# Kernel tuning notes

Hardware: AMD Instinct MI355X
Metric: run time of the kernel (lower is better)

Reference implementation:

```python
import jax, jax.numpy as jnp
import numpy as np

DIM = 256
NUM_HEADS = 8
HEAD_DIM = DIM // NUM_HEADS
NUM_MAIN = 2
NUM_MOD = 4
SEQ_MAIN = 1536
SEQ_AUX = 768
BS = 2


def setup_inputs() -> dict:
    key = jax.random.key(0)
    ks = jax.random.split(key, 6)
    x0 = jax.random.normal(ks[0], (BS, SEQ_MAIN, DIM), jnp.float32)
    x1 = jax.random.normal(ks[1], (BS, SEQ_MAIN, DIM), jnp.float32)
    x2 = jax.random.normal(ks[2], (BS, SEQ_AUX, DIM), jnp.float32)
    x3 = jax.random.normal(ks[3], (BS, SEQ_AUX, DIM), jnp.float32)
    Wqkv = jax.random.normal(ks[4], (NUM_MOD, DIM, 3 * DIM), jnp.float32) * 0.02
    bqkv = jnp.zeros((NUM_MOD, 3 * DIM), jnp.float32)
    Wproj = jax.random.normal(ks[5], (NUM_MOD, DIM, DIM), jnp.float32) * 0.02
    bproj = jnp.zeros((NUM_MOD, DIM), jnp.float32)
    return {"x0": x0, "x1": x1, "x2": x2, "x3": x3,
            "Wqkv": Wqkv, "bqkv": bqkv, "Wproj": Wproj, "bproj": bproj}


def _split_qkv(qkv):
    bs, s, _ = qkv.shape
    qkv = qkv.reshape(bs, s, 3, NUM_HEADS, HEAD_DIM).transpose(2, 0, 3, 1, 4)
    return qkv[0], qkv[1], qkv[2]


def _sdpa(q, k, v):
    scale = 1.0 / jnp.sqrt(jnp.asarray(HEAD_DIM, q.dtype))
    scores = jnp.einsum('bhqd,bhkd->bhqk', q, k) * scale
    probs = jax.nn.softmax(scores, axis=-1)
    return jnp.einsum('bhqk,bhkd->bhqd', probs, v)


def _merge_heads(t):
    # [bs, heads, s, head_dim] -> [bs, s, dim]
    bs, h, s, d = t.shape
    return t.transpose(0, 2, 1, 3).reshape(bs, s, h * d)


def reference(x0, x1, x2, x3, Wqkv, bqkv, Wproj, bproj):
    xs = [x0, x1, x2, x3]
    seqlens = [x.shape[1] for x in xs]
    qs, ks, vs = [], [], []
    for i in range(NUM_MOD):
        q, k, v = _split_qkv(xs[i] @ Wqkv[i] + bqkv[i])
        qs.append(q); ks.append(k); vs.append(v)

    main_q = jnp.concatenate(qs[:NUM_MAIN], axis=2)
    main_k = jnp.concatenate(ks[:NUM_MAIN], axis=2)
    main_v = jnp.concatenate(vs[:NUM_MAIN], axis=2)
    main_x = _merge_heads(_sdpa(main_q, main_k, main_v))  # [bs, sum(main seqlens), dim]
    splits = np.cumsum(seqlens[:NUM_MAIN])[:-1]
    outs = list(jnp.split(main_x, splits, axis=1))

    # aux modalities attend over detached main KV + own KV
    mk = jax.lax.stop_gradient(main_k)
    mv = jax.lax.stop_gradient(main_v)
    for i in range(NUM_MAIN, NUM_MOD):
        k = jnp.concatenate([mk, ks[i]], axis=2)
        v = jnp.concatenate([mv, vs[i]], axis=2)
        outs.append(_merge_heads(_sdpa(qs[i], k, v)))

    outs = [outs[i] @ Wproj[i] + bproj[i] for i in range(NUM_MOD)]
    # concatenate per-modality outputs along the sequence dim for a single output
    return jnp.concatenate(outs, axis=1)
```

## Files before the change

### kernel.cpp

```cpp
#include <hip/hip_runtime.h>
#include <hip/hip_bf16.h>
#include <math.h>

#define BS 2
#define NHEADS 8
#define HD 32
#define DIM 256
#define W3 768
#define S_MAIN 1536
#define S_AUX 768
#define SM_TOT 3072
#define S_TOT 4608

typedef _Float16 f16x8 __attribute__((ext_vector_type(8)));
typedef _Float16 f16x4 __attribute__((ext_vector_type(4)));
typedef float    f32x4 __attribute__((ext_vector_type(4)));

#define QK_SCALE 0.25503491f

#define QM_H  0
#define KM_H  1572864
#define VMT_H 3145728
#define QA_H  4718592
#define KA_H  5505024
#define VAT_H 6291456
#define AO0_F 3538944
#define AO1_F 5898240
#define L0_F  8257536
#define L1_F  8266752

#define GLOAD_LDS(SRC, DST)                                                    \
    __builtin_amdgcn_global_load_lds(                                          \
        (const __attribute__((address_space(1))) void*)(SRC),                  \
        (__attribute__((address_space(3))) void*)(DST), 16, 0, 0)

__global__ __launch_bounds__(256) void qkv_mfma_kernel(
    const float* __restrict__ x0, const float* __restrict__ x1,
    const float* __restrict__ x2, const float* __restrict__ x3,
    const float* __restrict__ Wqkv, const float* __restrict__ bqkv,
    _Float16* __restrict__ wsh)
{
    const int m  = blockIdx.z;
    const int rt = blockIdx.y;
    const int ct = blockIdx.x;
    const int s_m   = (m < 2) ? S_MAIN : S_AUX;
    const int nrows = BS * s_m;
    const int r0 = rt * 128;
    if (r0 >= nrows) return;

    const float* x    = (m == 0) ? x0 : (m == 1) ? x1 : (m == 2) ? x2 : x3;
    const float* W    = Wqkv + m * (DIM * W3);
    const float* bias = bqkv + m * W3;

    __shared__ _Float16 As[128][40];
    __shared__ _Float16 Bs[64][40];

    const int t    = threadIdx.x;
    const int wid  = t >> 6;
    const int lane = t & 63;
    const int g    = lane >> 4;
    const int c    = lane & 15;
    const int c0   = ct * 64;

    const int arow = t >> 1;
    const int ak   = (t & 1) << 4;
    const int bcol = t & 63;
    const int bkg  = t >> 6;
    const int bsg  = bkg ^ ((bcol >> 3) & 3);

    f32x4 acc[2][4];
    #pragma unroll
    for (int i = 0; i < 2; ++i)
        #pragma unroll
        for (int j = 0; j < 4; ++j)
            acc[i][j] = (f32x4){0.f, 0.f, 0.f, 0.f};

    const float* xp = x + (r0 + arow) * DIM + ak;
    const float* wp = W + (bkg * 8) * W3 + c0 + bcol;

    for (int kk = 0; kk < DIM; kk += 32) {
        {
            const float4 u0 = *(const float4*)(xp + kk + 0);
            const float4 u1 = *(const float4*)(xp + kk + 4);
            const float4 u2 = *(const float4*)(xp + kk + 8);
            const float4 u3 = *(const float4*)(xp + kk + 12);
            f16x8 h0, h1;
            h0[0] = (_Float16)u0.x; h0[1] = (_Float16)u0.y;
            h0[2] = (_Float16)u0.z; h0[3] = (_Float16)u0.w;
            h0[4] = (_Float16)u1.x; h0[5] = (_Float16)u1.y;
            h0[6] = (_Float16)u1.z; h0[7] = (_Float16)u1.w;
            h1[0] = (_Float16)u2.x; h1[1] = (_Float16)u2.y;
            h1[2] = (_Float16)u2.z; h1[3] = (_Float16)u2.w;
            h1[4] = (_Float16)u3.x; h1[5] = (_Float16)u3.y;
            h1[6] = (_Float16)u3.z; h1[7] = (_Float16)u3.w;
            *(f16x8*)&As[arow][ak]     = h0;
            *(f16x8*)&As[arow][ak + 8] = h1;
        }
        {
            const float* wq = wp + kk * W3;
            f16x8 hb;
            hb[0] = (_Float16)wq[0 * W3]; hb[1] = (_Float16)wq[1 * W3];
            hb[2] = (_Float16)wq[2 * W3]; hb[3] = (_Float16)wq[3 * W3];
            hb[4] = (_Float16)wq[4 * W3]; hb[5] = (_Float16)wq[5 * W3];
            hb[6] = (_Float16)wq[6 * W3]; hb[7] = (_Float16)wq[7 * W3];
            *(f16x8*)&Bs[bcol][bsg << 3] = hb;
        }
        __syncthreads();
        const f16x8 af0 = *(const f16x8*)&As[wid * 32 + c][g * 8];
        const f16x8 af1 = *(const f16x8*)&As[wid * 32 + 16 + c][g * 8];
        #pragma unroll
        for (int j = 0; j < 4; ++j) {
            const int bc = j * 16 + c;
            const int gg = g ^ ((bc >> 3) & 3);
            const f16x8 bf = *(const f16x8*)&Bs[bc][gg * 8];
            acc[0][j] = __builtin_amdgcn_mfma_f32_16x16x32_f16(af0, bf, acc[0][j], 0, 0, 0);
            acc[1][j] = __builtin_amdgcn_mfma_f32_16x16x32_f16(af1, bf, acc[1][j], 0, 0, 0);
        }
        __syncthreads();
    }

    #pragma unroll
    for (int i = 0; i < 2; ++i) {
        const int gr = r0 + wid * 32 + i * 16 + 4 * g;
        const int b  = (gr >= s_m) ? 1 : 0;
        const int s  = gr - (b ? s_m : 0);
        #pragma unroll
        for (int j = 0; j < 4; ++j) {
            const int col   = c0 + j * 16 + c;
            const int which = col >> 8;
            const int head  = (col >> 5) & 7;
            const int dd    = col & 31;
            const float bv  = bias[col];
            const f32x4 a   = acc[i][j];
            if (which < 2) {
                const float qs = (which == 0) ? QK_SCALE : 1.0f;
                _Float16* dst;
                int base;
                if (m < 2) {
                    dst  = wsh + (which == 0 ? QM_H : KM_H);
                    base = ((b * NHEADS + head) * SM_TOT + (s + m * S_MAIN)) * HD + dd;
                } else {
                    dst  = wsh + (which == 0 ? QA_H : KA_H);
                    base = ((((m - 2) * BS + b) * NHEADS + head) * S_AUX + s) * HD + dd;
                }
                dst[base + 0 * HD] = (_Float16)((a[0] + bv) * qs);
                dst[base + 1 * HD] = (_Float16)((a[1] + bv) * qs);
                dst[base + 2 * HD] = (_Float16)((a[2] + bv) * qs);
                dst[base + 3 * HD] = (_Float16)((a[3] + bv) * qs);
            } else {
                _Float16* dst;
                int base;
                if (m < 2) {
                    dst  = wsh + VMT_H;
                    base = ((b * NHEADS + head) * HD + dd) * SM_TOT + (s + m * S_MAIN);
                } else {
                    dst  = wsh + VAT_H;
                    base = ((((m - 2) * BS + b) * NHEADS + head) * HD + dd) * S_AUX + s;
                }
                f16x4 hv;
                hv[0] = (_Float16)(a[0] + bv);
                hv[1] = (_Float16)(a[1] + bv);
                hv[2] = (_Float16)(a[2] + bv);
                hv[3] = (_Float16)(a[3] + bv);
                *(f16x4*)(dst + base) = hv;
            }
        }
    }
}

__global__ __launch_bounds__(256) void attn_mfma_kernel(
    const _Float16* __restrict__ wsh, float* __restrict__ wsf)
{
    __shared__ _Float16 kbuf[2][64 * 32];
    __shared__ _Float16 vbuf[2][32 * 64];

    const int wid  = threadIdx.x >> 6;
    const int lane = threadIdx.x & 63;
    const int g    = lane >> 4;
    const int c    = lane & 15;

    const int bid = blockIdx.x;

    const _Float16 *qp, *kp0, *vt0, *kp1, *vt1;
    int n0, n1, vs1, orow0, ocol, half;

    if (bid < 384) {
        const int mbhg = bid / 12;
        const int mod  = mbhg >> 4;
        const int b    = (mbhg >> 3) & 1;
        const int h    = mbhg & 7;
        const int t    = bid % 12;
        const int qt   = t >> 1;
        half = t & 1;
        const int q0   = qt * 128 + wid * 32;
        const int mbh  = (mod * BS + b) * NHEADS + h;
        const int bh   = b * NHEADS + h;
        qp = wsh + QA_H + (mbh * S_AUX + q0) * HD;
        if (half == 0) {
            kp0 = wsh + KM_H  + bh * SM_TOT * HD;
            vt0 = wsh + VMT_H + bh * HD * SM_TOT;
            n0  = 1920;
            kp1 = nullptr; vt1 = nullptr; n1 = 0; vs1 = 0;
        } else {
            kp0 = wsh + KM_H  + (bh * SM_TOT + 1920) * HD;
            vt0 = wsh + VMT_H + bh * HD * SM_TOT + 1920;
            n0  = 1152;
            kp1 = wsh + KA_H  + mbh * S_AUX * HD;
            vt1 = wsh + VAT_H + mbh * HD * S_AUX;
            n1  = S_AUX; vs1 = S_AUX;
        }
        orow0 = b * S_TOT + SM_TOT + mod * S_AUX + q0;
        ocol  = h * HD;
    } else {
        const int idx = bid - 384;
        const int bh  = idx / 48;
        const int t   = idx % 48;
        const int qt  = t >> 1;
        half = t & 1;
        const int q0  = qt * 128 + wid * 32;
        const int b = bh >> 3, h = bh & 7;
        const int ks = half * 1536;
        qp  = wsh + QM_H  + (bh * SM_TOT + q0) * HD;
        kp0 = wsh + KM_H  + (bh * SM_TOT + ks) * HD;
        vt0 = wsh + VMT_H + bh * HD * SM_TOT + ks;
        n0  = 1536;
        kp1 = nullptr; vt1 = nullptr; n1 = 0; vs1 = 0;
        orow0 = b * S_TOT + q0;
        ocol  = h * HD;
    }

    const f16x8 qfA = *(const f16x8*)(qp + c * HD + g * 8);
    const f16x8 qfB = *(const f16x8*)(qp + (16 + c) * HD + g * 8);

    const int pc    = ((c >> 2) << 3) + (c & 3);
    const int koff0 = pc * HD + g * 8;
    const int koff1 = (pc + 4) * HD + g * 8;

    const int srow = wid * 8 + (lane >> 3);
    const int jl   = lane & 7;
    const int vswz = (jl ^ (srow & 7)) << 3;
    const int vr0 = ((g     ^ (c & 7)) << 3);
    const int vr1 = (((g+4) ^ (c & 7)) << 3);

    f16x8 ones;
    #pragma unroll
    for (int i = 0; i < 8; ++i) ones[i] = (_Float16)1.0f;

    f32x4 otA0 = {0.f, 0.f, 0.f, 0.f}, otA1 = {0.f, 0.f, 0.f, 0.f};
    f32x4 otB0 = {0.f, 0.f, 0.f, 0.f}, otB1 = {0.f, 0.f, 0.f, 0.f};
    f32x4 ltA  = {0.f, 0.f, 0.f, 0.f}, ltB  = {0.f, 0.f, 0.f, 0.f};

    int cur = 0;

    #pragma unroll 1
    for (int seg = 0; seg < 2; ++seg) {
        const _Float16* kp_ = seg ? kp1 : kp0;
        const _Float16* vt_ = seg ? vt1 : vt0;
        const int n  = seg ? n1  : n0;
        const int vs = seg ? vs1 : SM_TOT;
        if (n == 0) break;

        #define STAGE(BI, K0)                                                  \
            {                                                                  \
                const _Float16* ks_ = kp_ + (K0) * HD + wid * 512 + lane * 8;  \
                GLOAD_LDS(ks_, &kbuf[BI][wid * 512]);                          \
                const _Float16* vs_ = vt_ + (K0) + srow * vs + vswz;           \
                GLOAD_LDS(vs_, &vbuf[BI][wid * 512]);                          \
            }

        #define COMPUTE_TILE(BI)                                               \
            {                                                                  \
                const _Float16* kb_ = &kbuf[BI][0];                            \
                const _Float16* vb_ = &vbuf[BI][0];                            \
                const f16x8 kf0 = *(const f16x8*)(kb_ + koff0);                \
                const f16x8 kf1 = *(const f16x8*)(kb_ + koff1);                \
                const f16x8 kf2 = *(const f16x8*)(kb_ + 32 * HD + koff0);      \
                const f16x8 kf3 = *(const f16x8*)(kb_ + 32 * HD + koff1);      \
                const f16x8 va0 = *(const f16x8*)(vb_ + c * 64 + vr0);         \
                const f16x8 va1 = *(const f16x8*)(vb_ + (16 + c) * 64 + vr0);  \
                const f16x8 vb0 = *(const f16x8*)(vb_ + c * 64 + vr1);         \
                const f16x8 vb1 = *(const f16x8*)(vb_ + (16 + c) * 64 + vr1);  \
                f32x4 sA0 = __builtin_amdgcn_mfma_f32_16x16x32_f16(            \
                    kf0, qfA, (f32x4){0.f, 0.f, 0.f, 0.f}, 0, 0, 0);           \
                f32x4 sA1 = __builtin_amdgcn_mfma_f32_16x16x32_f16(            \
                    kf1, qfA, (f32x4){0.f, 0.f, 0.f, 0.f}, 0, 0, 0);           \
                f32x4 sA2 = __builtin_amdgcn_mfma_f32_16x16x32_f16(            \
                    kf2, qfA, (f32x4){0.f, 0.f, 0.f, 0.f}, 0, 0, 0);           \
                f32x4 sA3 = __builtin_amdgcn_mfma_f32_16x16x32_f16(            \
                    kf3, qfA, (f32x4){0.f, 0.f, 0.f, 0.f}, 0, 0, 0);           \
                f32x4 sB0 = __builtin_amdgcn_mfma_f32_16x16x32_f16(            \
                    kf0, qfB, (f32x4){0.f, 0.f, 0.f, 0.f}, 0, 0, 0);           \
                f32x4 sB1 = __builtin_amdgcn_mfma_f32_16x16x32_f16(            \
                    kf1, qfB, (f32x4){0.f, 0.f, 0.f, 0.f}, 0, 0, 0);           \
                f32x4 sB2 = __builtin_amdgcn_mfma_f32_16x16x32_f16(            \
                    kf2, qfB, (f32x4){0.f, 0.f, 0.f, 0.f}, 0, 0, 0);           \
                f32x4 sB3 = __builtin_amdgcn_mfma_f32_16x16x32_f16(            \
                    kf3, qfB, (f32x4){0.f, 0.f, 0.f, 0.f}, 0, 0, 0);           \
                float pA0[4], pA1[4], pA2[4], pA3[4];                          \
                float pB0[4], pB1[4], pB2[4], pB3[4];                          \
                _Pragma("unroll")                                              \
                for (int r = 0; r < 4; ++r) {                                  \
                    pA0[r] = __builtin_amdgcn_exp2f(sA0[r]);                   \
                    pA1[r] = __builtin_amdgcn_exp2f(sA1[r]);                   \
                    pA2[r] = __builtin_amdgcn_exp2f(sA2[r]);                   \
                    pA3[r] = __builtin_amdgcn_exp2f(sA3[r]);                   \
                    pB0[r] = __builtin_amdgcn_exp2f(sB0[r]);                   \
                    pB1[r] = __builtin_amdgcn_exp2f(sB1[r]);                   \
                    pB2[r] = __builtin_amdgcn_exp2f(sB2[r]);                   \
                    pB3[r] = __builtin_amdgcn_exp2f(sB3[r]);                   \
                }                                                              \
                f16x8 pbA0, pbA1, pbB0, pbB1;                                  \
                _Pragma("unroll")                                              \
                for (int r = 0; r < 4; ++r) {                                  \
                    pbA0[r]     = (_Float16)pA0[r];                            \
                    pbA0[r + 4] = (_Float16)pA1[r];                            \
                    pbA1[r]     = (_Float16)pA2[r];                            \
                    pbA1[r + 4] = (_Float16)pA3[r];                            \
                    pbB0[r]     = (_Float16)pB0[r];                            \
                    pbB0[r + 4] = (_Float16)pB1[r];                            \
                    pbB1[r]     = (_Float16)pB2[r];                            \
                    pbB1[r + 4] = (_Float16)pB3[r];                            \
                }                                                              \
                ltA = __builtin_amdgcn_mfma_f32_16x16x32_f16(ones, pbA0, ltA, 0, 0, 0); \
                ltA = __builtin_amdgcn_mfma_f32_16x16x32_f16(ones, pbA1, ltA, 0, 0, 0); \
                ltB = __builtin_amdgcn_mfma_f32_16x16x32_f16(ones, pbB0, ltB, 0, 0, 0); \
                ltB = __builtin_amdgcn_mfma_f32_16x16x32_f16(ones, pbB1, ltB, 0, 0, 0); \
                otA0 = __builtin_amdgcn_mfma_f32_16x16x32_f16(va0, pbA0, otA0, 0, 0, 0); \
                otA1 = __builtin_amdgcn_mfma_f32_16x16x32_f16(va1, pbA0, otA1, 0, 0, 0); \
                otB0 = __builtin_amdgcn_mfma_f32_16x16x32_f16(va0, pbB0, otB0, 0, 0, 0); \
                otB1 = __builtin_amdgcn_mfma_f32_16x16x32_f16(va1, pbB0, otB1, 0, 0, 0); \
                otA0 = __builtin_amdgcn_mfma_f32_16x16x32_f16(vb0, pbA1, otA0, 0, 0, 0); \
                otA1 = __builtin_amdgcn_mfma_f32_16x16x32_f16(vb1, pbA1, otA1, 0, 0, 0); \
                otB0 = __builtin_amdgcn_mfma_f32_16x16x32_f16(vb0, pbB1, otB0, 0, 0, 0); \
                otB1 = __builtin_amdgcn_mfma_f32_16x16x32_f16(vb1, pbB1, otB1, 0, 0, 0); \
            }

        STAGE(cur, 0);
        __syncthreads();

        #pragma unroll 1
        for (int k0 = 0; k0 < n; k0 += 64) {
            if (k0 + 64 < n)
                STAGE(cur ^ 1, k0 + 64);
            COMPUTE_TILE(cur);
            __syncthreads();
            cur ^= 1;
        }

        #undef STAGE
        #undef COMPUTE_TILE
    }

    float* aoBase = wsf + (half ? AO1_F : AO0_F);
    float* lBase  = wsf + (half ? L1_F  : L0_F);

    float* aoA = aoBase + (orow0 + c) * DIM + ocol;
    float* aoB = aoBase + (orow0 + 16 + c) * DIM + ocol;
    float4 w0, w1, w2, w3;
    w0.x = otA0[0]; w0.y = otA0[1]; w0.z = otA0[2]; w0.w = otA0[3];
    w1.x = otA1[0]; w1.y = otA1[1]; w1.z = otA1[2]; w1.w = otA1[3];
    w2.x = otB0[0]; w2.y = otB0[1]; w2.z = otB0[2]; w2.w = otB0[3];
    w3.x = otB1[0]; w3.y = otB1[1]; w3.z = otB1[2]; w3.w = otB1[3];
    *(float4*)(aoA + 4 * g)      = w0;
    *(float4*)(aoA + 16 + 4 * g) = w1;
    *(float4*)(aoB + 4 * g)      = w2;
    *(float4*)(aoB + 16 + 4 * g) = w3;

    if (g == 0) {
        lBase[orow0 + c]      = ltA[0];
        lBase[orow0 + 16 + c] = ltB[0];
    }
}

__global__ __launch_bounds__(256) void proj_mfma_kernel(
    const float* __restrict__ wsf, const float* __restrict__ Wproj,
    const float* __restrict__ bproj, float* __restrict__ out)
{
    const int ct = blockIdx.x;
    const int rt = blockIdx.y;
    const int r0 = rt * 128, c0 = ct * 64;
    const int seq = r0 % S_TOT;
    const int mod = (seq < S_MAIN) ? 0 : (seq < SM_TOT) ? 1
                  : (seq < SM_TOT + S_AUX) ? 2 : 3;
    const float* W    = Wproj + mod * DIM * DIM;
    const float* bias = bproj + mod * DIM;
    const float* A0   = wsf + AO0_F;
    const float* A1   = wsf + AO1_F;
    const float* L0p  = wsf + L0_F;
    const float* L1p  = wsf + L1_F;

    __shared__ _Float16 As[128][40];
    __shared__ _Float16 Bs[64][40];
    __shared__ float Linv[128];

    const int t    = threadIdx.x;
    const int wid  = t >> 6;
    const int lane = t & 63;
    const int g    = lane >> 4;
    const int c    = lane & 15;

    if (t < 128) Linv[t] = 1.0f / (L0p[r0 + t] + L1p[r0 + t]);
    __syncthreads();

    const int arow = t >> 1;
    const int ak   = (t & 1) << 4;
    const int bcol = t & 63;
    const int bkg  = t >> 6;
    const int bsg  = bkg ^ ((bcol >> 3) & 3);
    const float linv_r = Linv[arow];

    f32x4 acc[2][4];
    #pragma unroll
    for (int i = 0; i < 2; ++i)
        #pragma unroll
        for (int j = 0; j < 4; ++j)
            acc[i][j] = (f32x4){0.f, 0.f, 0.f, 0.f};

    const float* pa0 = A0 + (r0 + arow) * DIM + ak;
    const float* pa1 = A1 + (r0 + arow) * DIM + ak;
    const float* wp  = W + (bkg * 8) * DIM + c0 + bcol;

    for (int kk = 0; kk < DIM; kk += 32) {
        {
            const float4 u0 = *(const float4*)(pa0 + kk + 0);
            const float4 u1 = *(const float4*)(pa0 + kk + 4);
            const float4 u2 = *(const float4*)(pa0 + kk + 8);
            const float4 u3 = *(const float4*)(pa0 + kk + 12);
            const float4 v0 = *(const float4*)(pa1 + kk + 0);
            const float4 v1 = *(const float4*)(pa1 + kk + 4);
            const float4 v2 = *(const float4*)(pa1 + kk + 8);
            const float4 v3 = *(const float4*)(pa1 + kk + 12);
            f16x8 h0, h1;
            h0[0] = (_Float16)((u0.x + v0.x) * linv_r);
            h0[1] = (_Float16)((u0.y + v0.y) * linv_r);
            h0[2] = (_Float16)((u0.z + v0.z) * linv_r);
            h0[3] = (_Float16)((u0.w + v0.w) * linv_r);
            h0[4] = (_Float16)((u1.x + v1.x) * linv_r);
            h0[5] = (_Float16)((u1.y + v1.y) * linv_r);
            h0[6] = (_Float16)((u1.z + v1.z) * linv_r);
            h0[7] = (_Float16)((u1.w + v1.w) * linv_r);
            h1[0] = (_Float16)((u2.x + v2.x) * linv_r);
            h1[1] = (_Float16)((u2.y + v2.y) * linv_r);
            h1[2] = (_Float16)((u2.z + v2.z) * linv_r);
            h1[3] = (_Float16)((u2.w + v2.w) * linv_r);
            h1[4] = (_Float16)((u3.x + v3.x) * linv_r);
            h1[5] = (_Float16)((u3.y + v3.y) * linv_r);
            h1[6] = (_Float16)((u3.z + v3.z) * linv_r);
            h1[7] = (_Float16)((u3.w + v3.w) * linv_r);
            *(f16x8*)&As[arow][ak]     = h0;
            *(f16x8*)&As[arow][ak + 8] = h1;
        }
        {
            const float* wq = wp + kk * DIM;
            f16x8 hb;
            hb[0] = (_Float16)wq[0 * DIM]; hb[1] = (_Float16)wq[1 * DIM];
            hb[2] = (_Float16)wq[2 * DIM]; hb[3] = (_Float16)wq[3 * DIM];
            hb[4] = (_Float16)wq[4 * DIM]; hb[5] = (_Float16)wq[5 * DIM];
            hb[6] = (_Float16)wq[6 * DIM]; hb[7] = (_Float16)wq[7 * DIM];
            *(f16x8*)&Bs[bcol][bsg << 3] = hb;
        }
        __syncthreads();
        const f16x8 af0 = *(const f16x8*)&As[wid * 32 + c][g * 8];
        const f16x8 af1 = *(const f16x8*)&As[wid * 32 + 16 + c][g * 8];
        #pragma unroll
        for (int j = 0; j < 4; ++j) {
            const int bc = j * 16 + c;
            const int gg = g ^ ((bc >> 3) & 3);
            const f16x8 bf = *(const f16x8*)&Bs[bc][gg * 8];
            acc[0][j] = __builtin_amdgcn_mfma_f32_16x16x32_f16(af0, bf, acc[0][j], 0, 0, 0);
            acc[1][j] = __builtin_amdgcn_mfma_f32_16x16x32_f16(af1, bf, acc[1][j], 0, 0, 0);
        }
        __syncthreads();
    }

    #pragma unroll
    for (int i = 0; i < 2; ++i) {
        const int gr = r0 + wid * 32 + i * 16 + 4 * g;
        #pragma unroll
        for (int j = 0; j < 4; ++j) {
            const int col  = c0 + j * 16 + c;
            const float bv = bias[col];
            const f32x4 a  = acc[i][j];
            out[(gr + 0) * DIM + col] = a[0] + bv;
            out[(gr + 1) * DIM + col] = a[1] + bv;
            out[(gr + 2) * DIM + col] = a[2] + bv;
            out[(gr + 3) * DIM + col] = a[3] + bv;
        }
    }
}

extern "C" void kernel_launch(void* const* d_in, const int* in_sizes, int n_in,
                              void* d_out, int out_size, void* d_ws, size_t ws_size,
                              hipStream_t stream)
{
    const float* x0    = (const float*)d_in[0];
    const float* x1    = (const float*)d_in[1];
    const float* x2    = (const float*)d_in[2];
    const float* x3    = (const float*)d_in[3];
    const float* Wqkv  = (const float*)d_in[4];
    const float* bqkv  = (const float*)d_in[5];
    const float* Wproj = (const float*)d_in[6];
    const float* bproj = (const float*)d_in[7];
    _Float16* wsh = (_Float16*)d_ws;
    float*    wsf = (float*)d_ws;
    float*    out = (float*)d_out;

    qkv_mfma_kernel<<<dim3(12, 24, 4), 256, 0, stream>>>(
        x0, x1, x2, x3, Wqkv, bqkv, wsh);

    attn_mfma_kernel<<<dim3(1152), 256, 0, stream>>>(wsh, wsf);

    proj_mfma_kernel<<<dim3(4, 72), 256, 0, stream>>>(wsf, Wproj, bproj, out);
}
```

Before: 95.72 us.

## Pre-convert inputs and transpose weights to fp16, swizzle K tile loads in attention

Adds a conversion kernel that casts the activations to fp16 and writes transposed fp16 copies of the QKV and projection weights into workspace. The QKV and projection GEMMs then issue contiguous 16-byte fp16 loads in place of strided scalar fp32 weight reads and in-loop conversions. The attention kernel also applies an XOR swizzle to K tile staging to reduce LDS bank conflicts. In exchange it costs an extra kernel launch and an extra pass over x and the weights through global memory, and the weight transpose loop writes scalar fp16 values with a strided pattern.

```diff
diff --git a/kernel.cpp b/kernel.cpp
--- a/kernel.cpp
+++ b/kernel.cpp
@@ -24,20 +24,77 @@
 #define QA_H  4718592
 #define KA_H  5505024
 #define VAT_H 6291456
+#define XH_H  7077888
 #define AO0_F 3538944
 #define AO1_F 5898240
 #define L0_F  8257536
 #define L1_F  8266752
+#define WT1_H 16551936
+#define WT2_H 17338368
 
 #define GLOAD_LDS(SRC, DST)                                                    \
     __builtin_amdgcn_global_load_lds(                                          \
         (const __attribute__((address_space(1))) void*)(SRC),                  \
         (__attribute__((address_space(3))) void*)(DST), 16, 0, 0)
 
-__global__ __launch_bounds__(256) void qkv_mfma_kernel(
+__global__ __launch_bounds__(256) void convert_kernel(
     const float* __restrict__ x0, const float* __restrict__ x1,
     const float* __restrict__ x2, const float* __restrict__ x3,
-    const float* __restrict__ Wqkv, const float* __restrict__ bqkv,
+    const float* __restrict__ Wqkv, const float* __restrict__ Wproj,
+    _Float16* __restrict__ wsh)
+{
+    const int bid = blockIdx.x;
+    const int t   = threadIdx.x;
+
+    if (bid < 1152) {
+        const float* src;
+        int off;
+        if (bid < 384)      { src = x0; off = (bid      ) * 2048; }
+        else if (bid < 768) { src = x1 - 786432 + 0;  off = bid * 2048; }
+        else if (bid < 960) { src = x2; off = 1572864 + (bid - 768) * 2048; }
+        else                { src = x3; off = 1966080 + (bid - 960) * 2048; }
+        const int base = (bid < 384) ? bid * 2048
+                       : (bid < 768) ? (bid - 384) * 2048
+                       : (bid < 960) ? (bid - 768) * 2048
+                       : (bid - 960) * 2048;
+        const float* p = ((bid < 384) ? x0 : (bid < 768) ? x1
+                         : (bid < 960) ? x2 : x3) + base + t * 8;
+        _Float16* dst = wsh + XH_H + off + t * 8;
+        const float4 u0 = *(const float4*)(p + 0);
+        const float4 u1 = *(const float4*)(p + 4);
+        f16x8 h;
+        h[0] = (_Float16)u0.x; h[1] = (_Float16)u0.y;
+        h[2] = (_Float16)u0.z; h[3] = (_Float16)u0.w;
+        h[4] = (_Float16)u1.x; h[5] = (_Float16)u1.y;
+        h[6] = (_Float16)u1.z; h[7] = (_Float16)u1.w;
+        *(f16x8*)dst = h;
+    } else if (bid < 1200) {
+        const int i  = bid - 1152;
+        const int m  = i / 12;
+        const int cc = i % 12;
+        const int col = cc * 64 + (t & 63);
+        const int kq  = t >> 6;
+        const float* Wm = Wqkv + m * (DIM * W3);
+        _Float16*   Wt  = wsh + WT1_H + m * (W3 * DIM) + col * DIM;
+        #pragma unroll 4
+        for (int k = kq * 64; k < kq * 64 + 64; ++k)
+            Wt[k] = (_Float16)Wm[k * W3 + col];
+    } else {
+        const int i  = bid - 1200;
+        const int m  = i / 4;
+        const int cc = i % 4;
+        const int col = cc * 64 + (t & 63);
+        const int kq  = t >> 6;
+        const float* Wm = Wproj + m * (DIM * DIM);
+        _Float16*   Wt  = wsh + WT2_H + m * (DIM * DIM) + col * DIM;
+        #pragma unroll 4
+        for (int k = kq * 64; k < kq * 64 + 64; ++k)
+            Wt[k] = (_Float16)Wm[k * DIM + col];
+    }
+}
+
+__global__ __launch_bounds__(256) void qkv_mfma_kernel(
+    const _Float16* __restrict__ wsh_ro, const float* __restrict__ bqkv,
     _Float16* __restrict__ wsh)
 {
     const int m  = blockIdx.z;
@@ -48,9 +105,11 @@
     const int r0 = rt * 128;
     if (r0 >= nrows) return;
 
-    const float* x    = (m == 0) ? x0 : (m == 1) ? x1 : (m == 2) ? x2 : x3;
-    const float* W    = Wqkv + m * (DIM * W3);
-    const float* bias = bqkv + m * W3;
+    const int xoff = (m == 0) ? 0 : (m == 1) ? 786432
+                   : (m == 2) ? 1572864 : 1966080;
+    const _Float16* xh = wsh_ro + XH_H + xoff;
+    const _Float16* Wt = wsh_ro + WT1_H + m * (W3 * DIM);
+    const float* bias  = bqkv + m * W3;
 
     __shared__ _Float16 As[128][40];
     __shared__ _Float16 Bs[64][40];
@@ -75,34 +134,18 @@
         for (int j = 0; j < 4; ++j)
             acc[i][j] = (f32x4){0.f, 0.f, 0.f, 0.f};
 
-    const float* xp = x + (r0 + arow) * DIM + ak;
-    const float* wp = W + (bkg * 8) * W3 + c0 + bcol;
+    const _Float16* xp = xh + (r0 + arow) * DIM + ak;
+    const _Float16* wp = Wt + (c0 + bcol) * DIM;
 
     for (int kk = 0; kk < DIM; kk += 32) {
         {
-            const float4 u0 = *(const float4*)(xp + kk + 0);
-            const float4 u1 = *(const float4*)(xp + kk + 4);
-            const float4 u2 = *(const float4*)(xp + kk + 8);
-            const float4 u3 = *(const float4*)(xp + kk + 12);
-            f16x8 h0, h1;
-            h0[0] = (_Float16)u0.x; h0[1] = (_Float16)u0.y;
-            h0[2] = (_Float16)u0.z; h0[3] = (_Float16)u0.w;
-            h0[4] = (_Float16)u1.x; h0[5] = (_Float16)u1.y;
-            h0[6] = (_Float16)u1.z; h0[7] = (_Float16)u1.w;
-            h1[0] = (_Float16)u2.x; h1[1] = (_Float16)u2.y;
-            h1[2] = (_Float16)u2.z; h1[3] = (_Float16)u2.w;
-            h1[4] = (_Float16)u3.x; h1[5] = (_Float16)u3.y;
-            h1[6] = (_Float16)u3.z; h1[7] = (_Float16)u3.w;
+            const f16x8 h0 = *(const f16x8*)(xp + kk);
+            const f16x8 h1 = *(const f16x8*)(xp + kk + 8);
             *(f16x8*)&As[arow][ak]     = h0;
             *(f16x8*)&As[arow][ak + 8] = h1;
         }
         {
-            const float* wq = wp + kk * W3;
-            f16x8 hb;
-            hb[0] = (_Float16)wq[0 * W3]; hb[1] = (_Float16)wq[1 * W3];
-            hb[2] = (_Float16)wq[2 * W3]; hb[3] = (_Float16)wq[3 * W3];
-            hb[4] = (_Float16)wq[4 * W3]; hb[5] = (_Float16)wq[5 * W3];
-            hb[6] = (_Float16)wq[6 * W3]; hb[7] = (_Float16)wq[7 * W3];
+            const f16x8 hb = *(const f16x8*)(wp + kk + bkg * 8);
             *(f16x8*)&Bs[bcol][bsg << 3] = hb;
         }
         __syncthreads();
@@ -233,8 +276,12 @@
     const f16x8 qfB = *(const f16x8*)(qp + (16 + c) * HD + g * 8);
 
     const int pc    = ((c >> 2) << 3) + (c & 3);
-    const int koff0 = pc * HD + g * 8;
-    const int koff1 = (pc + 4) * HD + g * 8;
+    const int kchr  = (g ^ (c >> 2)) << 3;
+    const int koff0 = pc * HD + kchr;
+    const int koff1 = (pc + 4) * HD + kchr;
+
+    const int krow  = wid * 16 + (lane >> 2);
+    const int kchg  = ((lane & 3) ^ ((krow >> 3) & 3)) << 3;
 
     const int srow = wid * 8 + (lane >> 3);
     const int jl   = lane & 7;
@@ -262,7 +309,7 @@
 
         #define STAGE(BI, K0)                                                  \
             {                                                                  \
-                const _Float16* ks_ = kp_ + (K0) * HD + wid * 512 + lane * 8;  \
+                const _Float16* ks_ = kp_ + (K0 + krow) * HD + kchg;           \
                 GLOAD_LDS(ks_, &kbuf[BI][wid * 512]);                          \
                 const _Float16* vs_ = vt_ + (K0) + srow * vs + vswz;           \
                 GLOAD_LDS(vs_, &vbuf[BI][wid * 512]);                          \
@@ -373,7 +420,7 @@
 }
 
 __global__ __launch_bounds__(256) void proj_mfma_kernel(
-    const float* __restrict__ wsf, const float* __restrict__ Wproj,
+    const float* __restrict__ wsf, const _Float16* __restrict__ wsh_ro,
     const float* __restrict__ bproj, float* __restrict__ out)
 {
     const int ct = blockIdx.x;
@@ -382,12 +429,12 @@
     const int seq = r0 % S_TOT;
     const int mod = (seq < S_MAIN) ? 0 : (seq < SM_TOT) ? 1
                   : (seq < SM_TOT + S_AUX) ? 2 : 3;
-    const float* W    = Wproj + mod * DIM * DIM;
-    const float* bias = bproj + mod * DIM;
-    const float* A0   = wsf + AO0_F;
-    const float* A1   = wsf + AO1_F;
-    const float* L0p  = wsf + L0_F;
-    const float* L1p  = wsf + L1_F;
+    const _Float16* Wt = wsh_ro + WT2_H + mod * (DIM * DIM);
+    const float* bias  = bproj + mod * DIM;
+    const float* A0    = wsf + AO0_F;
+    const float* A1    = wsf + AO1_F;
+    const float* L0p   = wsf + L0_F;
+    const float* L1p   = wsf + L1_F;
 
     __shared__ _Float16 As[128][40];
     __shared__ _Float16 Bs[64][40];
@@ -418,7 +465,7 @@
 
     const float* pa0 = A0 + (r0 + arow) * DIM + ak;
     const float* pa1 = A1 + (r0 + arow) * DIM + ak;
-    const float* wp  = W + (bkg * 8) * DIM + c0 + bcol;
+    const _Float16* wp = Wt + (c0 + bcol) * DIM;
 
     for (int kk = 0; kk < DIM; kk += 32) {
         {
@@ -451,12 +498,7 @@
             *(f16x8*)&As[arow][ak + 8] = h1;
         }
         {
-            const float* wq = wp + kk * DIM;
-            f16x8 hb;
-            hb[0] = (_Float16)wq[0 * DIM]; hb[1] = (_Float16)wq[1 * DIM];
-            hb[2] = (_Float16)wq[2 * DIM]; hb[3] = (_Float16)wq[3 * DIM];
-            hb[4] = (_Float16)wq[4 * DIM]; hb[5] = (_Float16)wq[5 * DIM];
-            hb[6] = (_Float16)wq[6 * DIM]; hb[7] = (_Float16)wq[7 * DIM];
+            const f16x8 hb = *(const f16x8*)(wp + kk + bkg * 8);
             *(f16x8*)&Bs[bcol][bsg << 3] = hb;
         }
         __syncthreads();
@@ -505,10 +547,12 @@
     float*    wsf = (float*)d_ws;
     float*    out = (float*)d_out;
 
-    qkv_mfma_kernel<<<dim3(12, 24, 4), 256, 0, stream>>>(
-        x0, x1, x2, x3, Wqkv, bqkv, wsh);
+    convert_kernel<<<dim3(1216), 256, 0, stream>>>(
+        x0, x1, x2, x3, Wqkv, Wproj, wsh);
+
+    qkv_mfma_kernel<<<dim3(12, 24, 4), 256, 0, stream>>>(wsh, bqkv, wsh);
 
     attn_mfma_kernel<<<dim3(1152), 256, 0, stream>>>(wsh, wsf);
 
-    proj_mfma_kernel<<<dim3(4, 72), 256, 0, stream>>>(wsf, Wproj, bproj, out);
+    proj_mfma_kernel<<<dim3(4, 72), 256, 0, stream>>>(wsf, wsh, bproj, out);
 }
```

After: 101.7 us. 6.3% more time.

## Stage two 64-key tiles per barrier and XOR-swizzle K rows in LDS

Applied to the files above, without the earlier changes.

The attention loop now loads and computes two 64-key sub-tiles per double-buffer stage, so it hits one __syncthreads per 128 keys instead of per 64. K tiles are now written to LDS with an XOR-swizzled 16-byte chunk layout, and the fragment read offsets are adjusted to match, to cut LDS bank conflicts. LDS use doubles to 32 KB per block, which may lower occupancy. The loop assumes every segment length is a multiple of 128.

```diff
diff --git a/kernel.cpp b/kernel.cpp
--- a/kernel.cpp
+++ b/kernel.cpp
@@ -171,8 +171,8 @@
 __global__ __launch_bounds__(256) void attn_mfma_kernel(
     const _Float16* __restrict__ wsh, float* __restrict__ wsf)
 {
-    __shared__ _Float16 kbuf[2][64 * 32];
-    __shared__ _Float16 vbuf[2][32 * 64];
+    __shared__ _Float16 kbuf[2][2][64 * 32];
+    __shared__ _Float16 vbuf[2][2][32 * 64];
 
     const int wid  = threadIdx.x >> 6;
     const int lane = threadIdx.x & 63;
@@ -233,8 +233,12 @@
     const f16x8 qfB = *(const f16x8*)(qp + (16 + c) * HD + g * 8);
 
     const int pc    = ((c >> 2) << 3) + (c & 3);
-    const int koff0 = pc * HD + g * 8;
-    const int koff1 = (pc + 4) * HD + g * 8;
+    const int kchr  = (g ^ (c >> 2)) << 3;
+    const int koff0 = pc * HD + kchr;
+    const int koff1 = (pc + 4) * HD + kchr;
+
+    const int krow  = wid * 16 + (lane >> 2);
+    const int kchg  = ((lane & 3) ^ ((krow >> 3) & 3)) << 3;
 
     const int srow = wid * 8 + (lane >> 3);
     const int jl   = lane & 7;
@@ -260,18 +264,18 @@
         const int vs = seg ? vs1 : SM_TOT;
         if (n == 0) break;
 
-        #define STAGE(BI, K0)                                                  \
+        #define STAGE(BI, S, K0)                                               \
             {                                                                  \
-                const _Float16* ks_ = kp_ + (K0) * HD + wid * 512 + lane * 8;  \
-                GLOAD_LDS(ks_, &kbuf[BI][wid * 512]);                          \
+                const _Float16* ks_ = kp_ + (K0 + krow) * HD + kchg;           \
+                GLOAD_LDS(ks_, &kbuf[BI][S][wid * 512]);                       \
                 const _Float16* vs_ = vt_ + (K0) + srow * vs + vswz;           \
-                GLOAD_LDS(vs_, &vbuf[BI][wid * 512]);                          \
+                GLOAD_LDS(vs_, &vbuf[BI][S][wid * 512]);                       \
             }
 
-        #define COMPUTE_TILE(BI)                                               \
+        #define COMPUTE_TILE(BI, S)                                            \
             {                                                                  \
-                const _Float16* kb_ = &kbuf[BI][0];                            \
-                const _Float16* vb_ = &vbuf[BI][0];                            \
+                const _Float16* kb_ = &kbuf[BI][S][0];                         \
+                const _Float16* vb_ = &vbuf[BI][S][0];                         \
                 const f16x8 kf0 = *(const f16x8*)(kb_ + koff0);                \
                 const f16x8 kf1 = *(const f16x8*)(kb_ + koff1);                \
                 const f16x8 kf2 = *(const f16x8*)(kb_ + 32 * HD + koff0);      \
@@ -335,14 +339,18 @@
                 otB1 = __builtin_amdgcn_mfma_f32_16x16x32_f16(vb1, pbB1, otB1, 0, 0, 0); \
             }
 
-        STAGE(cur, 0);
+        STAGE(cur, 0, 0);
+        STAGE(cur, 1, 64);
         __syncthreads();
 
         #pragma unroll 1
-        for (int k0 = 0; k0 < n; k0 += 64) {
-            if (k0 + 64 < n)
-                STAGE(cur ^ 1, k0 + 64);
-            COMPUTE_TILE(cur);
+        for (int k0 = 0; k0 < n; k0 += 128) {
+            if (k0 + 128 < n) {
+                STAGE(cur ^ 1, 0, k0 + 128);
+                STAGE(cur ^ 1, 1, k0 + 192);
+            }
+            COMPUTE_TILE(cur, 0);
+            COMPUTE_TILE(cur, 1);
             __syncthreads();
             cur ^= 1;
         }
```

Result: faster. 91.95 us, median of 2 (-3.9%).
